# Optimization experiments

Hardware: AMD Instinct MI355X
Metric: run time of the kernel (lower is better)

## Reference

```python
import jax, jax.numpy as jnp
import numpy as np

D_IN = 32
K = 16


def cbr(x, W, s, b):
    # 1x1 Conv2d + folded (eval-mode) BatchNorm + ReLU, channels-last.
    return jax.nn.relu(jnp.einsum('...i,io->...o', x, W) * s + b)


def gather_neighbour(pc, idx):
    # pc: [B, N, d]; idx: [B, N, K] -> [B, N, K, d]
    B, N, d = pc.shape
    g = jnp.take_along_axis(pc, idx.reshape(B, -1, 1), axis=1)
    return g.reshape(B, N, K, d)


def setup_inputs() -> dict:
    key = jax.random.key(0)
    ks = jax.random.split(key, 32)
    B, N = 2, 65536

    def w(k, ci, co):
        return jax.random.normal(k, (ci, co), jnp.float32) * (1.0 / np.sqrt(ci))

    inp = {
        'feature': jax.random.normal(ks[0], (B, D_IN, N, 1), jnp.float32),
        'xyz': jax.random.normal(ks[1], (B, N, 3), jnp.float32),
        'neigh_idx': jax.random.randint(ks[2], (B, N, K), 0, N, jnp.int64),
        # TNet
        'tW1': w(ks[3], 3, 16),  'ts1': jnp.ones(16),  'tb1': jnp.zeros(16),
        'tW2': w(ks[4], 16, 64), 'ts2': jnp.ones(64),  'tb2': jnp.zeros(64),
        'tW3': w(ks[5], 64, 16), 'ts3': jnp.ones(16),  'tb3': jnp.zeros(16),
        'tW4': w(ks[6], 16, 9),  'tb4': jnp.zeros(9),
        # RFA mlps
        'W1': w(ks[7], 3, 3),            's1': jnp.ones(3),     'b1': jnp.zeros(3),
        'W2': w(ks[8], D_IN, D_IN),      's2': jnp.ones(D_IN),  'b2': jnp.zeros(D_IN),
        'W3': w(ks[9], D_IN + 3, D_IN),  's3': jnp.ones(D_IN),  'b3': jnp.zeros(D_IN),
        'W4': w(ks[10], 2 * D_IN, D_IN), 's4': jnp.ones(D_IN),  'b4': jnp.zeros(D_IN),
    }
    return inp


def tnet(xyz, tW1, ts1, tb1, tW2, ts2, tb2, tW3, ts3, tb3, tW4, tb4):
    h = cbr(xyz, tW1, ts1, tb1)          # [B, N, 16]
    h = cbr(h, tW2, ts2, tb2)            # [B, N, 64]
    h = jnp.max(h, axis=1, keepdims=True)  # [B, 1, 64]
    h = cbr(h, tW3, ts3, tb3)            # [B, 1, 16]
    h = jnp.einsum('...i,io->...o', h, tW4) + tb4  # [B, 1, 9] (no bn/act)
    dia = jnp.eye(3, dtype=h.dtype).reshape(1, 1, 9)
    return (h + dia).reshape(-1, 3, 3)


def reference(feature, xyz, neigh_idx,
              tW1, ts1, tb1, tW2, ts2, tb2, tW3, ts3, tb3, tW4, tb4,
              W1, s1, b1, W2, s2, b2, W3, s3, b3, W4, s4, b4):
    # channels-last features [B, N, d_in]
    feat = feature.squeeze(-1).transpose(0, 2, 1)

    t = tnet(xyz, tW1, ts1, tb1, tW2, ts2, tb2, tW3, ts3, tb3, tW4, tb4)
    f_xyz = jnp.einsum('bni,bij->bnj', xyz, t)   # [B, N, 3]
    f_xyz = cbr(f_xyz, W1, s1, b1)               # [B, N, 3]
    f_xyz = gather_neighbour(f_xyz, neigh_idx)   # [B, N, K, 3]

    f_nei = cbr(feat, W2, s2, b2)                # [B, N, d]
    f_nei = gather_neighbour(f_nei, neigh_idx)   # [B, N, K, d]

    f_cat = jnp.concatenate([f_nei, f_xyz], axis=-1)  # [B, N, K, d+3]
    f_cat = cbr(f_cat, W3, s3, b3)               # [B, N, K, d]
    f_cat = jnp.max(f_cat, axis=2)               # max pooling over K -> [B, N, d]

    f = jnp.concatenate([feat, f_cat], axis=-1)  # [B, N, 2d]
    f = cbr(f, W4, s4, b4)                       # [B, N, d_in]
    return f.transpose(0, 2, 1)[..., None]       # [B, d_in, N, 1]
```

## Files before the change

kernel.cpp:

```cpp
#include <hip/hip_runtime.h>

#define NPTS   65536
#define TOTAL  (2 * NPTS)
#define NUNITS 1024

typedef __attribute__((ext_vector_type(8)))  short short8;
typedef __attribute__((ext_vector_type(16))) float float16;
union F8 { uint4 u; short8 s; };

#define WS_STRIPE 0
#define WS_T1A    8192
#define WS_T1B    (8192 + TOTAL * 64)
#define WS_T2     (8192 + TOTAL * 64 + TOTAL * 8)

__device__ __forceinline__ unsigned short f2bf(float x) {
    unsigned u = __float_as_uint(x);
    return (unsigned short)((u + 0x7FFFu + ((u >> 16) & 1u)) >> 16);
}
__device__ __forceinline__ unsigned pk2(float a, float b) {
    return (unsigned)f2bf(a) | ((unsigned)f2bf(b) << 16);
}
__device__ __forceinline__ float relu(float x) { return x > 0.f ? x : 0.f; }
__device__ __forceinline__ uint4 pk8(const float* e) {
    uint4 u;
    u.x = pk2(e[0], e[1]); u.y = pk2(e[2], e[3]);
    u.z = pk2(e[4], e[5]); u.w = pk2(e[6], e[7]);
    return u;
}
__device__ __forceinline__ float16 zero16() {
    float16 z;
#pragma unroll
    for (int i = 0; i < 16; i++) z[i] = 0.f;
    return z;
}

__global__ __launch_bounds__(256) void kP0(
    const float* __restrict__ feature, const float* __restrict__ xyz,
    const float* __restrict__ tW1, const float* __restrict__ ts1, const float* __restrict__ tb1,
    const float* __restrict__ tW2, const float* __restrict__ ts2, const float* __restrict__ tb2,
    const float* __restrict__ W2,  const float* __restrict__ s2,  const float* __restrict__ b2,
    char* ws)
{
    __shared__ float red[4][64];
    float* stripe       = (float*)(ws + WS_STRIPE);
    unsigned short* t1a = (unsigned short*)(ws + WS_T1A);
    unsigned short* t2  = (unsigned short*)(ws + WS_T2);
    const int lane = threadIdx.x & 63, wv = threadIdx.x >> 6;
    const int col = lane & 31, h = lane >> 5;
    const float16 z = zero16();
    const int u = blockIdx.x;
    const int b = u >> 9;
    float e[8];
    float aw0[8], aw1[8], aw2[8], bb[8];
#pragma unroll
    for (int j = 0; j < 8; j++) {
        int k = 8 * h + j; float s = ts1[k];
        aw0[j] = tW1[k] * s; aw1[j] = tW1[16 + k] * s; aw2[j] = tW1[32 + k] * s;
        bb[j] = tb1[k];
    }
    F8 bf0, bf1;
#pragma unroll
    for (int j = 0; j < 8; j++) e[j] = tW2[(8 * h + j) * 64 + col] * ts2[col];
    bf0.u = pk8(e);
#pragma unroll
    for (int j = 0; j < 8; j++) e[j] = tW2[(8 * h + j) * 64 + 32 + col] * ts2[32 + col];
    bf1.u = pk8(e);
    F8 a0, a1;
    float sc2 = s2[col];
#pragma unroll
    for (int j = 0; j < 8; j++) e[j] = W2[(8 * h + j) * 32 + col] * sc2;
    a0.u = pk8(e);
#pragma unroll
    for (int j = 0; j < 8; j++) e[j] = W2[(16 + 8 * h + j) * 32 + col] * sc2;
    a1.u = pk8(e);
    float b2v[16];
#pragma unroll
    for (int r = 0; r < 16; r++) b2v[r] = b2[(r & 3) + 8 * (r >> 2) + 4 * h];

    int base = u * 128 + wv * 32;
    const float* xp = xyz + (size_t)(base + col) * 3;
    float x0 = xp[0], x1 = xp[1], x2 = xp[2];
    float hv[8];
#pragma unroll
    for (int j = 0; j < 8; j++)
        hv[j] = relu(x0 * aw0[j] + x1 * aw1[j] + x2 * aw2[j] + bb[j]);
    F8 af; af.u = pk8(hv);
    float16 c0 = __builtin_amdgcn_mfma_f32_32x32x16_bf16(af.s, bf0.s, z, 0, 0, 0);
    float16 c1 = __builtin_amdgcn_mfma_f32_32x32x16_bf16(af.s, bf1.s, z, 0, 0, 0);
    float v0 = c0[0], v1 = c1[0];
#pragma unroll
    for (int i = 1; i < 16; i++) { v0 = fmaxf(v0, c0[i]); v1 = fmaxf(v1, c1[i]); }
    v0 = fmaxf(v0, __shfl_xor(v0, 32));
    v1 = fmaxf(v1, __shfl_xor(v1, 32));
    if (h == 0) { red[wv][col] = v0; red[wv][32 + col] = v1; }
    __syncthreads();
    if (threadIdx.x < 64) {
        int c = threadIdx.x;
        float m = fmaxf(fmaxf(red[0][c], red[1][c]), fmaxf(red[2][c], red[3][c]));
        float val = relu(m + tb2[c]);
        atomicMax((unsigned*)(stripe + (u & 15) * 128 + b * 64 + c), __float_as_uint(val));
    }
    int pt = base + col;
    const float* fb = feature + (size_t)b * 32 * NPTS + (pt & (NPTS - 1));
    float v[8];
    F8 f0, f1;
#pragma unroll
    for (int j = 0; j < 8; j++) v[j] = fb[(size_t)(8 * h + j) * NPTS];
    f0.u = pk8(v);
#pragma unroll
    for (int j = 0; j < 8; j++) v[j] = fb[(size_t)(16 + 8 * h + j) * NPTS];
    f1.u = pk8(v);
    *(uint4*)(t2 + (size_t)pt * 32 + 8 * h) = f0.u;
    *(uint4*)(t2 + (size_t)pt * 32 + 16 + 8 * h) = f1.u;
    float16 acc = z;
    acc = __builtin_amdgcn_mfma_f32_32x32x16_bf16(a0.s, f0.s, acc, 0, 0, 0);
    acc = __builtin_amdgcn_mfma_f32_32x32x16_bf16(a1.s, f1.s, acc, 0, 0, 0);
#pragma unroll
    for (int q = 0; q < 4; q++) {
        int r = 4 * q;
        uint2 uu;
        uu.x = pk2(relu(acc[r] + b2v[r]), relu(acc[r + 1] + b2v[r + 1]));
        uu.y = pk2(relu(acc[r + 2] + b2v[r + 2]), relu(acc[r + 3] + b2v[r + 3]));
        *(uint2*)(t1a + (size_t)pt * 32 + 8 * q + 4 * h) = uu;
    }
}

__global__ __launch_bounds__(256) void kP23(
    const int* __restrict__ nidx, const float* __restrict__ xyz,
    const float* __restrict__ tW3, const float* __restrict__ ts3, const float* __restrict__ tb3,
    const float* __restrict__ tW4, const float* __restrict__ tb4,
    const float* __restrict__ W1,  const float* __restrict__ s1,  const float* __restrict__ b1,
    const float* __restrict__ W3,  const float* __restrict__ s3,  const float* __restrict__ b3,
    const float* __restrict__ W4,  const float* __restrict__ s4,  const float* __restrict__ b4,
    char* ws, float* __restrict__ out)
{
    __shared__ unsigned short mld[128 * 36];
    const float* stripe = (const float*)(ws + WS_STRIPE);
    const unsigned short* t1a = (const unsigned short*)(ws + WS_T1A);
    const unsigned short* t2  = (const unsigned short*)(ws + WS_T2);
    const int lane = threadIdx.x & 63, wv = threadIdx.x >> 6;
    const int col = lane & 31, h = lane >> 5;
    const float16 z = zero16();

    int slot = blockIdx.x & 7, batch = slot >> 2;
    int grp = (blockIdx.x >> 3) * 4 + (slot & 3);
    int u = batch * 512 + grp;
    int base = u * 128;

    float hm = 0.f;
#pragma unroll
    for (int s = 0; s < 16; s++)
        hm = fmaxf(hm, stripe[s * 128 + batch * 64 + lane]);
    float vv[16];
    {
        const float4* trow = (const float4*)(tW3 + lane * 16);
#pragma unroll
        for (int q = 0; q < 4; q++) {
            float4 t4 = trow[q];
            vv[4 * q + 0] = hm * t4.x; vv[4 * q + 1] = hm * t4.y;
            vv[4 * q + 2] = hm * t4.z; vv[4 * q + 3] = hm * t4.w;
        }
    }
#pragma unroll
    for (int off = 1; off < 64; off <<= 1) {
#pragma unroll
        for (int c = 0; c < 16; c++) vv[c] += __shfl_xor(vv[c], off);
    }
    float T[9];
#pragma unroll
    for (int j = 0; j < 9; j++) T[j] = tb4[j];
#pragma unroll
    for (int c = 0; c < 16; c++) {
        float h3 = relu(vv[c] * ts3[c] + tb3[c]);
#pragma unroll
        for (int j = 0; j < 9; j++) T[j] += h3 * tW4[c * 9 + j];
    }
    T[0] += 1.f; T[4] += 1.f; T[8] += 1.f;
#pragma unroll
    for (int j = 0; j < 9; j++)
        T[j] = __uint_as_float(__builtin_amdgcn_readfirstlane(__float_as_uint(T[j])));

    float e[8];
    F8 w0, w1, w2, zf;
    zf.u.x = zf.u.y = zf.u.z = zf.u.w = 0u;
    float sc3 = s3[col];
#pragma unroll
    for (int j = 0; j < 8; j++) e[j] = W3[(8 * h + j) * 32 + col] * sc3;
    w0.u = pk8(e);
#pragma unroll
    for (int j = 0; j < 8; j++) e[j] = W3[(16 + 8 * h + j) * 32 + col] * sc3;
    w1.u = pk8(e);
    w2 = zf;
    if (h == 0) {
        float e2[8] = {0.f, 0.f, 0.f, 0.f, 0.f, 0.f, 0.f, 0.f};
#pragma unroll
        for (int j = 0; j < 3; j++) e2[j] = W3[(32 + j) * 32 + col] * sc3;
        w2.u = pk8(e2);
    }
    float b3v = b3[col];
    F8 aw[4];
    float sc4 = s4[col];
#pragma unroll
    for (int t = 0; t < 4; t++) {
#pragma unroll
        for (int j = 0; j < 8; j++) e[j] = W4[(16 * t + 8 * h + j) * 32 + col] * sc4;
        aw[t].u = pk8(e);
    }
    float b4v[16];
#pragma unroll
    for (int r = 0; r < 16; r++) b4v[r] = b4[(r & 3) + 8 * (r >> 2) + 4 * h];

    unsigned idxp[8];
#pragma unroll
    for (int i2 = 0; i2 < 8; i2++) {
        unsigned lo = (unsigned)nidx[(base + 2 * (wv * 16 + 2 * i2)) * 16 + col];
        unsigned hi = (unsigned)nidx[(base + 2 * (wv * 16 + 2 * i2 + 1)) * 16 + col];
        idxp[i2] = (lo & 0xffffu) | (hi << 16);
    }

    F8 na0, na1;
    float nx0 = 0.f, nx1 = 0.f, nx2 = 0.f;
    {
        unsigned row = idxp[0] & 0xffffu;
        size_t g = ((size_t)batch << 16) + row;
        const unsigned short* ap = t1a + g * 32;
        na0.u = *(const uint4*)(ap + 8 * h);
        na1.u = *(const uint4*)(ap + 16 + 8 * h);
        if (h == 0) {
            const float* xp = xyz + g * 3;
            nx0 = xp[0]; nx1 = xp[1]; nx2 = xp[2];
        }
    }
#pragma unroll
    for (int it = 0; it < 16; it++) {
        F8 ca0 = na0, ca1 = na1;
        float cx0 = nx0, cx1 = nx1, cx2 = nx2;
        if (it < 15) {
            unsigned row = (idxp[(it + 1) >> 1] >> (16 * ((it + 1) & 1))) & 0xffffu;
            size_t g = ((size_t)batch << 16) + row;
            const unsigned short* ap = t1a + g * 32;
            na0.u = *(const uint4*)(ap + 8 * h);
            na1.u = *(const uint4*)(ap + 16 + 8 * h);
            if (h == 0) {
                const float* xp = xyz + g * 3;
                nx0 = xp[0]; nx1 = xp[1]; nx2 = xp[2];
            }
        }
        F8 ca2 = zf;
        if (h == 0) {
            float q0 = cx0 * T[0] + cx1 * T[3] + cx2 * T[6];
            float q1 = cx0 * T[1] + cx1 * T[4] + cx2 * T[7];
            float q2 = cx0 * T[2] + cx1 * T[5] + cx2 * T[8];
            float r0 = relu((q0 * W1[0] + q1 * W1[3] + q2 * W1[6]) * s1[0] + b1[0]);
            float r1 = relu((q0 * W1[1] + q1 * W1[4] + q2 * W1[7]) * s1[1] + b1[1]);
            float r2 = relu((q0 * W1[2] + q1 * W1[5] + q2 * W1[8]) * s1[2] + b1[2]);
            ca2.u.x = pk2(r0, r1); ca2.u.y = pk2(r2, 0.f);
        }
        float16 acc = z;
        acc = __builtin_amdgcn_mfma_f32_32x32x16_bf16(ca0.s, w0.s, acc, 0, 0, 0);
        acc = __builtin_amdgcn_mfma_f32_32x32x16_bf16(ca1.s, w1.s, acc, 0, 0, 0);
        acc = __builtin_amdgcn_mfma_f32_32x32x16_bf16(ca2.s, w2.s, acc, 0, 0, 0);
        float vA = acc[0], vB = acc[8];
#pragma unroll
        for (int r = 1; r < 8; r++) { vA = fmaxf(vA, acc[r]); vB = fmaxf(vB, acc[8 + r]); }
        vA = fmaxf(vA, __shfl_xor(vA, 32));
        vB = fmaxf(vB, __shfl_xor(vB, 32));
        vA = relu(vA + b3v);
        vB = relu(vB + b3v);
        float val = h ? vB : vA;
        int pi = wv * 16 + it;
        mld[(2 * pi + h) * 36 + col] = f2bf(val);
    }

    int p_loc = wv * 32 + col;
    int p = base + p_loc;
    const unsigned short* bp = t2 + (size_t)p * 32 + 8 * h;
    F8 x0, x1, x2, x3;
    x0.u = *(const uint4*)(bp);
    x1.u = *(const uint4*)(bp + 16);
    const unsigned short* mp = mld + p_loc * 36;
    uint2 q0 = *(const uint2*)(mp + 8 * h);
    uint2 q1 = *(const uint2*)(mp + 8 * h + 4);
    uint2 q2 = *(const uint2*)(mp + 16 + 8 * h);
    uint2 q3 = *(const uint2*)(mp + 16 + 8 * h + 4);
    x2.u.x = q0.x; x2.u.y = q0.y; x2.u.z = q1.x; x2.u.w = q1.y;
    x3.u.x = q2.x; x3.u.y = q2.y; x3.u.z = q3.x; x3.u.w = q3.y;
    float16 acc = z;
    acc = __builtin_amdgcn_mfma_f32_32x32x16_bf16(aw[0].s, x0.s, acc, 0, 0, 0);
    acc = __builtin_amdgcn_mfma_f32_32x32x16_bf16(aw[1].s, x1.s, acc, 0, 0, 0);
    acc = __builtin_amdgcn_mfma_f32_32x32x16_bf16(aw[2].s, x2.s, acc, 0, 0, 0);
    acc = __builtin_amdgcn_mfma_f32_32x32x16_bf16(aw[3].s, x3.s, acc, 0, 0, 0);
    float* ob = out + (size_t)(batch * 32) * NPTS + (p & (NPTS - 1));
#pragma unroll
    for (int r = 0; r < 16; r++) {
        int o = (r & 3) + 8 * (r >> 2) + 4 * h;
        ob[(size_t)o * NPTS] = relu(acc[r] + b4v[r]);
    }
}

extern "C" void kernel_launch(void* const* d_in, const int* in_sizes, int n_in,
                              void* d_out, int out_size, void* d_ws, size_t ws_size,
                              hipStream_t stream)
{
    const float* feature = (const float*)d_in[0];
    const float* xyz     = (const float*)d_in[1];
    const int*   nidx    = (const int*)d_in[2];
    const float* tW1 = (const float*)d_in[3];
    const float* ts1 = (const float*)d_in[4];
    const float* tb1 = (const float*)d_in[5];
    const float* tW2 = (const float*)d_in[6];
    const float* ts2 = (const float*)d_in[7];
    const float* tb2 = (const float*)d_in[8];
    const float* tW3 = (const float*)d_in[9];
    const float* ts3 = (const float*)d_in[10];
    const float* tb3 = (const float*)d_in[11];
    const float* tW4 = (const float*)d_in[12];
    const float* tb4 = (const float*)d_in[13];
    const float* W1  = (const float*)d_in[14];
    const float* s1  = (const float*)d_in[15];
    const float* b1  = (const float*)d_in[16];
    const float* W2  = (const float*)d_in[17];
    const float* s2  = (const float*)d_in[18];
    const float* b2  = (const float*)d_in[19];
    const float* W3  = (const float*)d_in[20];
    const float* s3  = (const float*)d_in[21];
    const float* b3  = (const float*)d_in[22];
    const float* W4  = (const float*)d_in[23];
    const float* s4  = (const float*)d_in[24];
    const float* b4  = (const float*)d_in[25];
    (void)in_sizes; (void)n_in; (void)out_size; (void)ws_size;

    char* wsp = (char*)d_ws;
    float* outp = (float*)d_out;

    hipMemsetAsync(wsp + WS_STRIPE, 0, 16 * 128 * sizeof(float), stream);
    kP0<<<NUNITS, 256, 0, stream>>>(feature, xyz, tW1, ts1, tb1, tW2, ts2, tb2,
                                    W2, s2, b2, wsp);
    kP23<<<NUNITS, 256, 0, stream>>>(nidx, xyz, tW3, ts3, tb3, tW4, tb4,
                                     W1, s1, b1, W3, s3, b3, W4, s4, b4, wsp, outp);
}
```

Before: 163.7 us.

## Precompute W3 conv per point before gather, then max-pool gathered bf16 rows

The W3 conv with BN and ReLU now runs once per source point in a new kernel kP1h, which writes bf16 rows to workspace. The old path computed it for every one of the K gathered neighbours. kP23 now gathers those precomputed rows and max-reduces them with packed 16-bit integer max, which is valid because the values are non-negative bf16. This cuts MFMA work by a factor of K at the cost of an extra kernel launch and an extra workspace write and read.

```diff
diff --git a/kernel.cpp b/kernel.cpp
--- a/kernel.cpp
+++ b/kernel.cpp
@@ -12,6 +12,7 @@
 #define WS_T1A    8192
 #define WS_T1B    (8192 + TOTAL * 64)
 #define WS_T2     (8192 + TOTAL * 64 + TOTAL * 8)
+#define WS_H      (8192 + TOTAL * 64 + TOTAL * 8 + TOTAL * 64)
 
 __device__ __forceinline__ unsigned short f2bf(float x) {
     unsigned u = __float_as_uint(x);
@@ -32,6 +33,11 @@
 #pragma unroll
     for (int i = 0; i < 16; i++) z[i] = 0.f;
     return z;
+}
+__device__ __forceinline__ unsigned pkmax(unsigned a, unsigned b) {
+    unsigned d;
+    asm("v_pk_max_i16 %0, %1, %2" : "=v"(d) : "v"(a), "v"(b));
+    return d;
 }
 
 __global__ __launch_bounds__(256) void kP0(
@@ -125,27 +131,24 @@
     }
 }
 
-__global__ __launch_bounds__(256) void kP23(
-    const int* __restrict__ nidx, const float* __restrict__ xyz,
+__global__ __launch_bounds__(256) void kP1h(
+    const float* __restrict__ xyz,
     const float* __restrict__ tW3, const float* __restrict__ ts3, const float* __restrict__ tb3,
     const float* __restrict__ tW4, const float* __restrict__ tb4,
     const float* __restrict__ W1,  const float* __restrict__ s1,  const float* __restrict__ b1,
     const float* __restrict__ W3,  const float* __restrict__ s3,  const float* __restrict__ b3,
-    const float* __restrict__ W4,  const float* __restrict__ s4,  const float* __restrict__ b4,
-    char* ws, float* __restrict__ out)
+    char* ws)
 {
-    __shared__ unsigned short mld[128 * 36];
+    __shared__ unsigned short hst[128 * 40];
     const float* stripe = (const float*)(ws + WS_STRIPE);
     const unsigned short* t1a = (const unsigned short*)(ws + WS_T1A);
-    const unsigned short* t2  = (const unsigned short*)(ws + WS_T2);
+    unsigned short* hT = (unsigned short*)(ws + WS_H);
     const int lane = threadIdx.x & 63, wv = threadIdx.x >> 6;
     const int col = lane & 31, h = lane >> 5;
     const float16 z = zero16();
-
-    int slot = blockIdx.x & 7, batch = slot >> 2;
-    int grp = (blockIdx.x >> 3) * 4 + (slot & 3);
-    int u = batch * 512 + grp;
-    int base = u * 128;
+    const int u = blockIdx.x;
+    const int batch = u >> 9;
+    const int base = u * 128;
 
     float hm = 0.f;
 #pragma unroll
@@ -198,6 +201,99 @@
         w2.u = pk8(e2);
     }
     float b3v = b3[col];
+
+    int pt = base + wv * 32 + col;
+    const unsigned short* ap = t1a + (size_t)pt * 32;
+    F8 ca0, ca1;
+    ca0.u = *(const uint4*)(ap + 8 * h);
+    ca1.u = *(const uint4*)(ap + 16 + 8 * h);
+    const float* xp = xyz + (size_t)pt * 3;
+    float x0 = xp[0], x1 = xp[1], x2 = xp[2];
+    F8 ca2 = zf;
+    {
+        float q0 = x0 * T[0] + x1 * T[3] + x2 * T[6];
+        float q1 = x0 * T[1] + x1 * T[4] + x2 * T[7];
+        float q2 = x0 * T[2] + x1 * T[5] + x2 * T[8];
+        float r0 = relu((q0 * W1[0] + q1 * W1[3] + q2 * W1[6]) * s1[0] + b1[0]);
+        float r1 = relu((q0 * W1[1] + q1 * W1[4] + q2 * W1[7]) * s1[1] + b1[1]);
+        float r2 = relu((q0 * W1[2] + q1 * W1[5] + q2 * W1[8]) * s1[2] + b1[2]);
+        if (h == 0) { ca2.u.x = pk2(r0, r1); ca2.u.y = pk2(r2, 0.f); }
+        else        { ca2 = zf; }
+    }
+    float16 acc = z;
+    acc = __builtin_amdgcn_mfma_f32_32x32x16_bf16(ca0.s, w0.s, acc, 0, 0, 0);
+    acc = __builtin_amdgcn_mfma_f32_32x32x16_bf16(ca1.s, w1.s, acc, 0, 0, 0);
+    acc = __builtin_amdgcn_mfma_f32_32x32x16_bf16(ca2.s, w2.s, acc, 0, 0, 0);
+#pragma unroll
+    for (int r = 0; r < 16; r++) {
+        int row = (r & 3) + 8 * (r >> 2) + 4 * h;
+        hst[(wv * 32 + row) * 40 + col] = f2bf(relu(acc[r] + b3v));
+    }
+    int lr = lane >> 1, c2 = lane & 1;
+    int grow = wv * 32 + lr;
+    uint4 d0 = *(const uint4*)(hst + grow * 40 + 8 * c2);
+    uint4 d1 = *(const uint4*)(hst + grow * 40 + 16 + 8 * c2);
+    unsigned short* hrow = hT + (size_t)(base + grow) * 32;
+    *(uint4*)(hrow + 8 * c2) = d0;
+    *(uint4*)(hrow + 16 + 8 * c2) = d1;
+}
+
+__global__ __launch_bounds__(256) void kP23(
+    const int* __restrict__ nidx,
+    const float* __restrict__ W4, const float* __restrict__ s4, const float* __restrict__ b4,
+    char* ws, float* __restrict__ out)
+{
+    __shared__ unsigned short mld[128 * 40];
+    const unsigned short* t2 = (const unsigned short*)(ws + WS_T2);
+    const unsigned short* hT = (const unsigned short*)(ws + WS_H);
+    const int tid = threadIdx.x;
+    const int lane = tid & 63, wv = tid >> 6;
+    const int col = lane & 31, h = lane >> 5;
+    const float16 z = zero16();
+
+    int slot = blockIdx.x & 7, batch = slot >> 2;
+    int grp = (blockIdx.x >> 3) * 4 + (slot & 3);
+    int u = batch * 512 + grp;
+    int base = u * 128;
+
+    {
+        int p = tid >> 1, c2 = tid & 1;
+        const int4* ip = (const int4*)(nidx + (size_t)(base + p) * 16);
+        int4 I0 = ip[0], I1 = ip[1], I2 = ip[2], I3 = ip[3];
+        int idx[16] = { I0.x, I0.y, I0.z, I0.w, I1.x, I1.y, I1.z, I1.w,
+                        I2.x, I2.y, I2.z, I2.w, I3.x, I3.y, I3.z, I3.w };
+        const unsigned short* hbase = hT + (((size_t)batch << 16) * 32);
+        uint4 pfA[8], pfB[8];
+#pragma unroll
+        for (int k = 0; k < 8; k++) {
+            const unsigned short* hp = hbase + (size_t)(unsigned)idx[k] * 32;
+            pfA[k] = *(const uint4*)(hp + 8 * c2);
+            pfB[k] = *(const uint4*)(hp + 16 + 8 * c2);
+        }
+        unsigned m0 = 0u, m1 = 0u, m2 = 0u, m3 = 0u,
+                 m4 = 0u, m5 = 0u, m6 = 0u, m7 = 0u;
+#pragma unroll
+        for (int k = 0; k < 16; k++) {
+            const int s = k & 7;
+            uint4 A = pfA[s], B = pfB[s];
+            if (k + 8 < 16) {
+                const unsigned short* hp = hbase + (size_t)(unsigned)idx[k + 8] * 32;
+                pfA[s] = *(const uint4*)(hp + 8 * c2);
+                pfB[s] = *(const uint4*)(hp + 16 + 8 * c2);
+            }
+            m0 = pkmax(m0, A.x); m1 = pkmax(m1, A.y);
+            m2 = pkmax(m2, A.z); m3 = pkmax(m3, A.w);
+            m4 = pkmax(m4, B.x); m5 = pkmax(m5, B.y);
+            m6 = pkmax(m6, B.z); m7 = pkmax(m7, B.w);
+        }
+        uint4 wa, wb;
+        wa.x = m0; wa.y = m1; wa.z = m2; wa.w = m3;
+        wb.x = m4; wb.y = m5; wb.z = m6; wb.w = m7;
+        *(uint4*)(mld + p * 40 + 8 * c2) = wa;
+        *(uint4*)(mld + p * 40 + 16 + 8 * c2) = wb;
+    }
+
+    float e[8];
     F8 aw[4];
     float sc4 = s4[col];
 #pragma unroll
@@ -209,68 +305,6 @@
     float b4v[16];
 #pragma unroll
     for (int r = 0; r < 16; r++) b4v[r] = b4[(r & 3) + 8 * (r >> 2) + 4 * h];
-
-    unsigned idxp[8];
-#pragma unroll
-    for (int i2 = 0; i2 < 8; i2++) {
-        unsigned lo = (unsigned)nidx[(base + 2 * (wv * 16 + 2 * i2)) * 16 + col];
-        unsigned hi = (unsigned)nidx[(base + 2 * (wv * 16 + 2 * i2 + 1)) * 16 + col];
-        idxp[i2] = (lo & 0xffffu) | (hi << 16);
-    }
-
-    F8 na0, na1;
-    float nx0 = 0.f, nx1 = 0.f, nx2 = 0.f;
-    {
-        unsigned row = idxp[0] & 0xffffu;
-        size_t g = ((size_t)batch << 16) + row;
-        const unsigned short* ap = t1a + g * 32;
-        na0.u = *(const uint4*)(ap + 8 * h);
-        na1.u = *(const uint4*)(ap + 16 + 8 * h);
-        if (h == 0) {
-            const float* xp = xyz + g * 3;
-            nx0 = xp[0]; nx1 = xp[1]; nx2 = xp[2];
-        }
-    }
-#pragma unroll
-    for (int it = 0; it < 16; it++) {
-        F8 ca0 = na0, ca1 = na1;
-        float cx0 = nx0, cx1 = nx1, cx2 = nx2;
-        if (it < 15) {
-            unsigned row = (idxp[(it + 1) >> 1] >> (16 * ((it + 1) & 1))) & 0xffffu;
-            size_t g = ((size_t)batch << 16) + row;
-            const unsigned short* ap = t1a + g * 32;
-            na0.u = *(const uint4*)(ap + 8 * h);
-            na1.u = *(const uint4*)(ap + 16 + 8 * h);
-            if (h == 0) {
-                const float* xp = xyz + g * 3;
-                nx0 = xp[0]; nx1 = xp[1]; nx2 = xp[2];
-            }
-        }
-        F8 ca2 = zf;
-        if (h == 0) {
-            float q0 = cx0 * T[0] + cx1 * T[3] + cx2 * T[6];
-            float q1 = cx0 * T[1] + cx1 * T[4] + cx2 * T[7];
-            float q2 = cx0 * T[2] + cx1 * T[5] + cx2 * T[8];
-            float r0 = relu((q0 * W1[0] + q1 * W1[3] + q2 * W1[6]) * s1[0] + b1[0]);
-            float r1 = relu((q0 * W1[1] + q1 * W1[4] + q2 * W1[7]) * s1[1] + b1[1]);
-            float r2 = relu((q0 * W1[2] + q1 * W1[5] + q2 * W1[8]) * s1[2] + b1[2]);
-            ca2.u.x = pk2(r0, r1); ca2.u.y = pk2(r2, 0.f);
-        }
-        float16 acc = z;
-        acc = __builtin_amdgcn_mfma_f32_32x32x16_bf16(ca0.s, w0.s, acc, 0, 0, 0);
-        acc = __builtin_amdgcn_mfma_f32_32x32x16_bf16(ca1.s, w1.s, acc, 0, 0, 0);
-        acc = __builtin_amdgcn_mfma_f32_32x32x16_bf16(ca2.s, w2.s, acc, 0, 0, 0);
-        float vA = acc[0], vB = acc[8];
-#pragma unroll
-        for (int r = 1; r < 8; r++) { vA = fmaxf(vA, acc[r]); vB = fmaxf(vB, acc[8 + r]); }
-        vA = fmaxf(vA, __shfl_xor(vA, 32));
-        vB = fmaxf(vB, __shfl_xor(vB, 32));
-        vA = relu(vA + b3v);
-        vB = relu(vB + b3v);
-        float val = h ? vB : vA;
-        int pi = wv * 16 + it;
-        mld[(2 * pi + h) * 36 + col] = f2bf(val);
-    }
 
     int p_loc = wv * 32 + col;
     int p = base + p_loc;
@@ -278,7 +312,7 @@
     F8 x0, x1, x2, x3;
     x0.u = *(const uint4*)(bp);
     x1.u = *(const uint4*)(bp + 16);
-    const unsigned short* mp = mld + p_loc * 36;
+    const unsigned short* mp = mld + p_loc * 40;
     uint2 q0 = *(const uint2*)(mp + 8 * h);
     uint2 q1 = *(const uint2*)(mp + 8 * h + 4);
     uint2 q2 = *(const uint2*)(mp + 16 + 8 * h);
@@ -336,6 +370,7 @@
     hipMemsetAsync(wsp + WS_STRIPE, 0, 16 * 128 * sizeof(float), stream);
     kP0<<<NUNITS, 256, 0, stream>>>(feature, xyz, tW1, ts1, tb1, tW2, ts2, tb2,
                                     W2, s2, b2, wsp);
-    kP23<<<NUNITS, 256, 0, stream>>>(nidx, xyz, tW3, ts3, tb3, tW4, tb4,
-                                     W1, s1, b1, W3, s3, b3, W4, s4, b4, wsp, outp);
-}
+    kP1h<<<NUNITS, 256, 0, stream>>>(xyz, tW3, ts3, tb3, tW4, tb4,
+                                     W1, s1, b1, W3, s3, b3, wsp);
+    kP23<<<NUNITS, 256, 0, stream>>>(nidx, W4, s4, b4, wsp, outp);
+}
```

After: 156.8 us, median of 2. 4.2% less time.
